# Performance work log

Measured on AMD Instinct MI355X. Metric: run time of the kernel, lower is better.

The kernel has to match this reference:

```python
import jax, jax.numpy as jnp
import numpy as np


def _bilinear_ac(img, H, W):
    """Bilinear resize with align_corners=True. img: [B, C, h, w] -> [B, C, H, W]."""
    B, C, h, w = img.shape
    ys = jnp.linspace(0.0, h - 1.0, H)
    xs = jnp.linspace(0.0, w - 1.0, W)
    y0 = jnp.floor(ys).astype(jnp.int32)
    x0 = jnp.floor(xs).astype(jnp.int32)
    y1 = jnp.minimum(y0 + 1, h - 1)
    x1 = jnp.minimum(x0 + 1, w - 1)
    wy = (ys - y0).astype(img.dtype)  # [H]
    wx = (xs - x0).astype(img.dtype)  # [W]
    top = img[:, :, y0, :]            # [B, C, H, w]
    bot = img[:, :, y1, :]
    row = top * (1.0 - wy)[None, None, :, None] + bot * wy[None, None, :, None]
    left = row[:, :, :, x0]           # [B, C, H, W]
    right = row[:, :, :, x1]
    return left * (1.0 - wx)[None, None, None, :] + right * wx[None, None, None, :]


def setup_inputs() -> dict:
    key = jax.random.key(0)
    k1, k2, k3 = jax.random.split(key, 3)
    B, F, h, w = 16, 256, 64, 64
    H, W = 512, 512
    K = 21
    feature_map = jax.random.normal(k1, (B, F, h, w), dtype=jnp.float32)
    x = jax.random.uniform(k2, (B, 3, H, W), dtype=jnp.float32)
    conv_w = jax.random.normal(k3, (K, F), dtype=jnp.float32) * 0.05
    conv_b = jnp.zeros((K,), dtype=jnp.float32)
    return {"feature_map": feature_map, "x": x, "conv_w": conv_w, "conv_b": conv_b}


def reference(feature_map, x, conv_w, conv_b):
    B, _, H, W = x.shape
    # 1x1 conv: feature_dim -> num_classes
    logits = jnp.einsum('bfhw,kf->bkhw', feature_map, conv_w) + conv_b[None, :, None, None]
    seg = jax.nn.softmax(logits, axis=1)                 # [B, K, h, w]
    seg = _bilinear_ac(seg, H, W)                        # [B, K, H, W]
    xp = jnp.transpose(x, (0, 2, 3, 1))                  # [B, H, W, C]
    # per-class masked mean pooling (the python loop, fused into one einsum)
    q = jnp.einsum('bhwc,bkhw->bkc', xp, seg) / (H * W)  # [B, K, C]
    # broadcast dot-product attention maps
    attn = jnp.einsum('bhwc,bkc->bkhw', xp, q)           # [B, K, H, W]
    return attn
```

## Files before the change

kernel.cpp:

```cpp
#include <hip/hip_runtime.h>

#define BN 16
#define FD 256
#define SH 64
#define SW 64
#define BH 512
#define BW 512
#define KN 21
#define SP (SH*SW)
#define BP (BH*BW)

#define SEG_BLOCKS 64
#define DOWNX_BLOCKS (BN*3*BH*SW/256)

typedef float f32x4 __attribute__((ext_vector_type(4)));

__device__ __forceinline__ float adj_w(int big, int small) {
    double t = (double)big * (63.0 / 511.0);
    int i0 = (int)t;
    double fr = t - (double)i0;
    int i1 = i0 + 1; if (i1 > 63) i1 = 63;
    float w = 0.0f;
    if (i0 == small) w += (float)(1.0 - fr);
    if (i1 == small) w += (float)fr;
    return w;
}

__device__ __forceinline__ void adj_range(int small, int& lo, int& hi) {
    lo = (int)floorf((small - 1) * (511.0f / 63.0f)); if (lo < 0) lo = 0;
    hi = (int)ceilf((small + 1) * (511.0f / 63.0f));  if (hi > 511) hi = 511;
}

__device__ __forceinline__ void seg_body(int blk, int tid,
                                         const float* __restrict__ fm,
                                         const float* __restrict__ cw,
                                         const float* __restrict__ cb,
                                         float* __restrict__ seg) {
    int gid = blk * 256 + tid;
    int b   = gid >> 10;
    int p4  = gid & 1023;
    const f32x4* fmb = (const f32x4*)(fm + (size_t)b * FD * SP) + p4;

    f32x4 acc[KN];
#pragma unroll
    for (int k = 0; k < KN; ++k) acc[k] = (f32x4)0.0f;

#pragma unroll 2
    for (int f = 0; f < FD; ++f) {
        f32x4 v = fmb[f * (SP / 4)];
#pragma unroll
        for (int k = 0; k < KN; ++k)
            acc[k] += v * cw[k * FD + f];
    }

    f32x4 mx = (f32x4)(-1e30f);
#pragma unroll
    for (int k = 0; k < KN; ++k) {
        acc[k] += cb[k];
        mx.x = fmaxf(mx.x, acc[k].x); mx.y = fmaxf(mx.y, acc[k].y);
        mx.z = fmaxf(mx.z, acc[k].z); mx.w = fmaxf(mx.w, acc[k].w);
    }
    f32x4 s = (f32x4)0.0f;
#pragma unroll
    for (int k = 0; k < KN; ++k) {
        acc[k].x = expf(acc[k].x - mx.x); acc[k].y = expf(acc[k].y - mx.y);
        acc[k].z = expf(acc[k].z - mx.z); acc[k].w = expf(acc[k].w - mx.w);
        s += acc[k];
    }
    f32x4 inv;
    inv.x = 1.0f / s.x; inv.y = 1.0f / s.y; inv.z = 1.0f / s.z; inv.w = 1.0f / s.w;

    f32x4* segb = (f32x4*)(seg + (size_t)b * KN * SP) + p4;
#pragma unroll
    for (int k = 0; k < KN; ++k) segb[k * (SP / 4)] = acc[k] * inv;
}

__device__ __forceinline__ void downx_body(int blk, int tid,
                                           const float* __restrict__ x,
                                           float* __restrict__ tmpA) {
    int gid = blk * 256 + tid;
    int s  = gid & 63;
    int Y  = (gid >> 6) & 511;
    int bc = gid >> 15;
    const float* row = x + ((size_t)bc * BH + Y) * BW;
    int lo, hi; adj_range(s, lo, hi);
    float acc = 0.0f;
    for (int X = lo; X <= hi; ++X) acc = fmaf(adj_w(X, s), row[X], acc);
    tmpA[gid] = acc;
}

__global__ __launch_bounds__(256) void k_phase1(const float* __restrict__ fm,
                                                const float* __restrict__ cw,
                                                const float* __restrict__ cb,
                                                const float* __restrict__ x,
                                                float* __restrict__ seg,
                                                float* __restrict__ tmpA) {
    if (blockIdx.x < SEG_BLOCKS) seg_body(blockIdx.x, threadIdx.x, fm, cw, cb, seg);
    else                         downx_body(blockIdx.x - SEG_BLOCKS, threadIdx.x, x, tmpA);
}

__global__ __launch_bounds__(256) void k_downy(const float* __restrict__ tmpA,
                                               float* __restrict__ xd) {
    int gid = blockIdx.x * 256 + threadIdx.x;
    int s  = gid & 63;
    int r  = (gid >> 6) & 63;
    int bc = gid >> 12;
    const float* base = tmpA + (size_t)bc * BH * SW + s;
    int lo, hi; adj_range(r, lo, hi);
    float acc = 0.0f;
    for (int Y = lo; Y <= hi; ++Y) acc = fmaf(adj_w(Y, r), base[(size_t)Y * SW], acc);
    xd[gid] = acc;
}

__global__ __launch_bounds__(256) void k_q(const float* __restrict__ seg,
                                           const float* __restrict__ xd,
                                           float* __restrict__ q) {
    int b = blockIdx.x / KN, k = blockIdx.x % KN;
    const float* sg = seg + ((size_t)b * KN + k) * SP;
    const float* xb = xd + (size_t)b * 3 * SP;
    float a0 = 0.f, a1 = 0.f, a2 = 0.f;
    for (int p = threadIdx.x; p < SP; p += 256) {
        float sv = sg[p];
        a0 = fmaf(sv, xb[p], a0);
        a1 = fmaf(sv, xb[SP + p], a1);
        a2 = fmaf(sv, xb[2 * SP + p], a2);
    }
    __shared__ float red[3][256];
    red[0][threadIdx.x] = a0; red[1][threadIdx.x] = a1; red[2][threadIdx.x] = a2;
    __syncthreads();
    for (int off = 128; off > 0; off >>= 1) {
        if (threadIdx.x < (unsigned)off) {
            red[0][threadIdx.x] += red[0][threadIdx.x + off];
            red[1][threadIdx.x] += red[1][threadIdx.x + off];
            red[2][threadIdx.x] += red[2][threadIdx.x + off];
        }
        __syncthreads();
    }
    if (threadIdx.x == 0) {
        const float scale = 1.0f / (float)BP;
        float* qo = q + ((size_t)b * KN + k) * 3;
        qo[0] = red[0][0] * scale;
        qo[1] = red[1][0] * scale;
        qo[2] = red[2][0] * scale;
    }
}

__global__ __launch_bounds__(256) void k_attn(const float* __restrict__ x,
                                              const float* __restrict__ q,
                                              float* __restrict__ out) {
    int b   = blockIdx.x >> 8;
    int blk = blockIdx.x & 255;
    int p4  = blk * 256 + threadIdx.x;

    const f32x4* xb = (const f32x4*)(x + (size_t)b * 3 * BP);
    f32x4 x0 = xb[p4];
    f32x4 x1 = xb[BP / 4 + p4];
    f32x4 x2 = xb[2 * (BP / 4) + p4];

    __shared__ float qs[KN * 3];
    if (threadIdx.x < KN * 3) qs[threadIdx.x] = q[(size_t)b * KN * 3 + threadIdx.x];
    __syncthreads();

    f32x4* ob = (f32x4*)(out + (size_t)b * KN * BP) + p4;
#pragma unroll
    for (int k = 0; k < KN; ++k) {
        float q0 = qs[k * 3], q1 = qs[k * 3 + 1], q2 = qs[k * 3 + 2];
        f32x4 r = x0 * q0 + x1 * q1 + x2 * q2;
        __builtin_nontemporal_store(r, ob + (size_t)k * (BP / 4));
    }
}

extern "C" void kernel_launch(void* const* d_in, const int* in_sizes, int n_in,
                              void* d_out, int out_size, void* d_ws, size_t ws_size,
                              hipStream_t stream) {
    const float* fm = (const float*)d_in[0];
    const float* x  = (const float*)d_in[1];
    const float* cw = (const float*)d_in[2];
    const float* cb = (const float*)d_in[3];
    float* out = (float*)d_out;

    float* seg  = (float*)d_ws;
    float* tmpA = seg  + (size_t)BN * KN * SP;
    float* xd   = tmpA + (size_t)BN * 3 * BH * SW;
    float* q    = xd   + (size_t)BN * 3 * SP;

    k_phase1<<<SEG_BLOCKS + DOWNX_BLOCKS, 256, 0, stream>>>(fm, cw, cb, x, seg, tmpA);
    k_downy <<<BN * 3 * SP / 256,         256, 0, stream>>>(tmpA, xd);
    k_q     <<<BN * KN,                   256, 0, stream>>>(seg, xd, q);
    k_attn  <<<BN * (BP / 1024),          256, 0, stream>>>(x, q, out);
}
```

Before: 509.4 us.

## Fuse vertical downsample with q reduction and rework phase-1 seg and downx

Several changes land together. The seg 1x1-conv plus softmax now uses one pixel per thread over 256 blocks instead of float4 over 64 blocks, and the adjoint weights are computed in float instead of double. Horizontal downsampling stages four input rows in shared memory with vectorized loads. The vertical downsample is merged into the q reduction kernel, which runs one block per (batch, channel), removing the xd buffer and one launch, and uses wave shuffles for the reduction. The attention output store switches from nontemporal to a regular store. The fused q kernel launches only 48 blocks, which risks underusing the GPU.

```diff
diff --git a/kernel.cpp b/kernel.cpp
--- a/kernel.cpp
+++ b/kernel.cpp
@@ -10,19 +10,19 @@
 #define SP (SH*SW)
 #define BP (BH*BW)
 
-#define SEG_BLOCKS 64
-#define DOWNX_BLOCKS (BN*3*BH*SW/256)
+#define SEG_BLOCKS 256
+#define DOWNX_BLOCKS (BN*3*BH/4)
 
 typedef float f32x4 __attribute__((ext_vector_type(4)));
 
 __device__ __forceinline__ float adj_w(int big, int small) {
-    double t = (double)big * (63.0 / 511.0);
+    float t = (float)big * (63.0f / 511.0f);
     int i0 = (int)t;
-    double fr = t - (double)i0;
+    float fr = t - (float)i0;
     int i1 = i0 + 1; if (i1 > 63) i1 = 63;
     float w = 0.0f;
-    if (i0 == small) w += (float)(1.0 - fr);
-    if (i1 == small) w += (float)fr;
+    if (i0 == small) w += 1.0f - fr;
+    if (i1 == small) w += fr;
     return w;
 }
 
@@ -37,56 +37,53 @@
                                          const float* __restrict__ cb,
                                          float* __restrict__ seg) {
     int gid = blk * 256 + tid;
-    int b   = gid >> 10;
-    int p4  = gid & 1023;
-    const f32x4* fmb = (const f32x4*)(fm + (size_t)b * FD * SP) + p4;
+    int b   = gid >> 12;
+    int p   = gid & 4095;
+    const float* fmb = fm + (size_t)b * FD * SP + p;
 
-    f32x4 acc[KN];
+    float acc[KN];
 #pragma unroll
-    for (int k = 0; k < KN; ++k) acc[k] = (f32x4)0.0f;
+    for (int k = 0; k < KN; ++k) acc[k] = 0.0f;
 
-#pragma unroll 2
+#pragma unroll 4
     for (int f = 0; f < FD; ++f) {
-        f32x4 v = fmb[f * (SP / 4)];
+        float v = fmb[(size_t)f * SP];
 #pragma unroll
         for (int k = 0; k < KN; ++k)
-            acc[k] += v * cw[k * FD + f];
+            acc[k] = fmaf(v, cw[k * FD + f], acc[k]);
     }
 
-    f32x4 mx = (f32x4)(-1e30f);
+    float mx = -1e30f;
 #pragma unroll
-    for (int k = 0; k < KN; ++k) {
-        acc[k] += cb[k];
-        mx.x = fmaxf(mx.x, acc[k].x); mx.y = fmaxf(mx.y, acc[k].y);
-        mx.z = fmaxf(mx.z, acc[k].z); mx.w = fmaxf(mx.w, acc[k].w);
-    }
-    f32x4 s = (f32x4)0.0f;
+    for (int k = 0; k < KN; ++k) { acc[k] += cb[k]; mx = fmaxf(mx, acc[k]); }
+    float s = 0.0f;
 #pragma unroll
-    for (int k = 0; k < KN; ++k) {
-        acc[k].x = expf(acc[k].x - mx.x); acc[k].y = expf(acc[k].y - mx.y);
-        acc[k].z = expf(acc[k].z - mx.z); acc[k].w = expf(acc[k].w - mx.w);
-        s += acc[k];
-    }
-    f32x4 inv;
-    inv.x = 1.0f / s.x; inv.y = 1.0f / s.y; inv.z = 1.0f / s.z; inv.w = 1.0f / s.w;
+    for (int k = 0; k < KN; ++k) { acc[k] = expf(acc[k] - mx); s += acc[k]; }
+    float inv = 1.0f / s;
 
-    f32x4* segb = (f32x4*)(seg + (size_t)b * KN * SP) + p4;
+    float* segb = seg + (size_t)b * KN * SP + p;
 #pragma unroll
-    for (int k = 0; k < KN; ++k) segb[k * (SP / 4)] = acc[k] * inv;
+    for (int k = 0; k < KN; ++k) segb[(size_t)k * SP] = acc[k] * inv;
 }
 
 __device__ __forceinline__ void downx_body(int blk, int tid,
                                            const float* __restrict__ x,
-                                           float* __restrict__ tmpA) {
-    int gid = blk * 256 + tid;
-    int s  = gid & 63;
-    int Y  = (gid >> 6) & 511;
-    int bc = gid >> 15;
-    const float* row = x + ((size_t)bc * BH + Y) * BW;
+                                           float* __restrict__ tmpA,
+                                           float (*rows)[BW]) {
+    int bc = blk >> 7;
+    int Y0 = (blk & 127) << 2;
+    const f32x4* src = (const f32x4*)(x + ((size_t)bc * BH + Y0) * BW);
+    f32x4* dst = (f32x4*)&rows[0][0];
+    dst[tid]       = src[tid];
+    dst[tid + 256] = src[tid + 256];
+    __syncthreads();
+
+    int s  = tid & 63;
+    int yl = tid >> 6;
     int lo, hi; adj_range(s, lo, hi);
     float acc = 0.0f;
-    for (int X = lo; X <= hi; ++X) acc = fmaf(adj_w(X, s), row[X], acc);
-    tmpA[gid] = acc;
+    for (int X = lo; X <= hi; ++X) acc = fmaf(adj_w(X, s), rows[yl][X], acc);
+    tmpA[((size_t)bc * BH + Y0 + yl) * SW + s] = acc;
 }
 
 __global__ __launch_bounds__(256) void k_phase1(const float* __restrict__ fm,
@@ -95,53 +92,48 @@
                                                 const float* __restrict__ x,
                                                 float* __restrict__ seg,
                                                 float* __restrict__ tmpA) {
+    __shared__ float rows[4][BW];
     if (blockIdx.x < SEG_BLOCKS) seg_body(blockIdx.x, threadIdx.x, fm, cw, cb, seg);
-    else                         downx_body(blockIdx.x - SEG_BLOCKS, threadIdx.x, x, tmpA);
+    else                         downx_body(blockIdx.x - SEG_BLOCKS, threadIdx.x, x, tmpA, rows);
 }
 
-__global__ __launch_bounds__(256) void k_downy(const float* __restrict__ tmpA,
-                                               float* __restrict__ xd) {
-    int gid = blockIdx.x * 256 + threadIdx.x;
-    int s  = gid & 63;
-    int r  = (gid >> 6) & 63;
-    int bc = gid >> 12;
-    const float* base = tmpA + (size_t)bc * BH * SW + s;
-    int lo, hi; adj_range(r, lo, hi);
-    float acc = 0.0f;
-    for (int Y = lo; Y <= hi; ++Y) acc = fmaf(adj_w(Y, r), base[(size_t)Y * SW], acc);
-    xd[gid] = acc;
-}
+__global__ __launch_bounds__(256) void k_downyq(const float* __restrict__ tmpA,
+                                                const float* __restrict__ seg,
+                                                float* __restrict__ q) {
+    int bc = blockIdx.x;
+    int b  = bc / 3, c = bc - b * 3;
+    const float* base = tmpA + (size_t)bc * BH * SW;
+    const float* segb = seg + (size_t)b * KN * SP;
 
-__global__ __launch_bounds__(256) void k_q(const float* __restrict__ seg,
-                                           const float* __restrict__ xd,
-                                           float* __restrict__ q) {
-    int b = blockIdx.x / KN, k = blockIdx.x % KN;
-    const float* sg = seg + ((size_t)b * KN + k) * SP;
-    const float* xb = xd + (size_t)b * 3 * SP;
-    float a0 = 0.f, a1 = 0.f, a2 = 0.f;
-    for (int p = threadIdx.x; p < SP; p += 256) {
-        float sv = sg[p];
-        a0 = fmaf(sv, xb[p], a0);
-        a1 = fmaf(sv, xb[SP + p], a1);
-        a2 = fmaf(sv, xb[2 * SP + p], a2);
+    float qk[KN];
+#pragma unroll
+    for (int k = 0; k < KN; ++k) qk[k] = 0.0f;
+
+    for (int i = 0; i < SP / 256; ++i) {
+        int p = i * 256 + threadIdx.x;
+        int r = p >> 6, s = p & 63;
+        int lo, hi; adj_range(r, lo, hi);
+        float xv = 0.0f;
+        for (int Y = lo; Y <= hi; ++Y)
+            xv = fmaf(adj_w(Y, r), base[(size_t)Y * SW + s], xv);
+#pragma unroll
+        for (int k = 0; k < KN; ++k)
+            qk[k] = fmaf(segb[(size_t)k * SP + p], xv, qk[k]);
     }
-    __shared__ float red[3][256];
-    red[0][threadIdx.x] = a0; red[1][threadIdx.x] = a1; red[2][threadIdx.x] = a2;
+
+    __shared__ float red[4][KN];
+    int lane = threadIdx.x & 63, w = threadIdx.x >> 6;
+#pragma unroll
+    for (int k = 0; k < KN; ++k) {
+        float v = qk[k];
+        for (int off = 32; off > 0; off >>= 1) v += __shfl_down(v, off, 64);
+        if (lane == 0) red[w][k] = v;
+    }
     __syncthreads();
-    for (int off = 128; off > 0; off >>= 1) {
-        if (threadIdx.x < (unsigned)off) {
-            red[0][threadIdx.x] += red[0][threadIdx.x + off];
-            red[1][threadIdx.x] += red[1][threadIdx.x + off];
-            red[2][threadIdx.x] += red[2][threadIdx.x + off];
-        }
-        __syncthreads();
-    }
-    if (threadIdx.x == 0) {
-        const float scale = 1.0f / (float)BP;
-        float* qo = q + ((size_t)b * KN + k) * 3;
-        qo[0] = red[0][0] * scale;
-        qo[1] = red[1][0] * scale;
-        qo[2] = red[2][0] * scale;
+    if (threadIdx.x < KN) {
+        float v = red[0][threadIdx.x] + red[1][threadIdx.x]
+                + red[2][threadIdx.x] + red[3][threadIdx.x];
+        q[((size_t)b * KN + threadIdx.x) * 3 + c] = v * (1.0f / (float)BP);
     }
 }
 
@@ -166,7 +158,7 @@
     for (int k = 0; k < KN; ++k) {
         float q0 = qs[k * 3], q1 = qs[k * 3 + 1], q2 = qs[k * 3 + 2];
         f32x4 r = x0 * q0 + x1 * q1 + x2 * q2;
-        __builtin_nontemporal_store(r, ob + (size_t)k * (BP / 4));
+        ob[(size_t)k * (BP / 4)] = r;
     }
 }
 
@@ -181,11 +173,9 @@
 
     float* seg  = (float*)d_ws;
     float* tmpA = seg  + (size_t)BN * KN * SP;
-    float* xd   = tmpA + (size_t)BN * 3 * BH * SW;
-    float* q    = xd   + (size_t)BN * 3 * SP;
+    float* q    = tmpA + (size_t)BN * 3 * BH * SW;
 
     k_phase1<<<SEG_BLOCKS + DOWNX_BLOCKS, 256, 0, stream>>>(fm, cw, cb, x, seg, tmpA);
-    k_downy <<<BN * 3 * SP / 256,         256, 0, stream>>>(tmpA, xd);
-    k_q     <<<BN * KN,                   256, 0, stream>>>(seg, xd, q);
+    k_downyq<<<BN * 3,                    256, 0, stream>>>(tmpA, seg, q);
     k_attn  <<<BN * (BP / 1024),          256, 0, stream>>>(x, q, out);
 }
```

Result: slower. 565.0 us (+10.9%).
